# Kernel optimization log

Hardware: AMD Instinct MI355X
Metric: run time of the kernel (lower is better)

## Reference

```python
import jax, jax.numpy as jnp
import numpy as np

LOWER = 300  # hidden size of the critic MLP


def setup_inputs() -> dict:
    key = jax.random.key(0)
    ks = jax.random.split(key, 6)
    N, XD, YD = 1024, 768, 768
    x = jax.random.normal(ks[0], (N, XD), dtype=jnp.float32)
    y = jax.random.normal(ks[1], (N, YD), dtype=jnp.float32)
    # Linear(x_dim+y_dim -> LOWER), Linear(LOWER -> 1); Kaiming-uniform-ish init
    b1_lim = 1.0 / np.sqrt(XD + YD)
    b2_lim = 1.0 / np.sqrt(LOWER)
    W1 = jax.random.uniform(ks[2], (XD + YD, LOWER), jnp.float32, -b1_lim, b1_lim)
    b1 = jax.random.uniform(ks[3], (LOWER,), jnp.float32, -b1_lim, b1_lim)
    W2 = jax.random.uniform(ks[4], (LOWER, 1), jnp.float32, -b2_lim, b2_lim)
    b2 = jax.random.uniform(ks[5], (1,), jnp.float32, -b2_lim, b2_lim)
    return {"x_samples": x, "y_samples": y, "W1": W1, "b1": b1, "W2": W2, "b2": b2}


def reference(x_samples, y_samples, W1, b1, W2, b2):
    N = y_samples.shape[0]
    xd = x_samples.shape[-1]
    # Decompose first Linear: cat([x, y]) @ W1 == x @ W1[:xd] + y @ W1[xd:]
    Wx, Wy = W1[:xd], W1[xd:]
    hx = x_samples @ Wx          # [N, LOWER]
    hy = y_samples @ Wy          # [N, LOWER]
    w2 = W2[:, 0]                # [LOWER]

    def critic(h):
        # relu -> Linear(LOWER->1) -> softplus
        return jax.nn.softplus(jax.nn.relu(h) @ w2 + b2[0])

    # T0[i] = F(x[i], y[i])
    T0 = critic(hx + hy + b1)                       # [N]
    # T1[i, j] = F(x[j], y[i])  (x tiled over dim 0, y over dim 1)
    h_pair = hy[:, None, :] + hx[None, :, :] + b1   # [N, N, LOWER]
    T1 = critic(h_pair)                             # [N, N]
    lower_bound = (T0.mean()
                   - jax.nn.logsumexp(T1, axis=1).mean()
                   - jnp.log(jnp.float32(N)))
    return lower_bound
```

## Files before the change

kernel.cpp:

```cpp
#include <hip/hip_runtime.h>
#include <math.h>

#define N_S  1024
#define XD   768
#define LOW  300
#define KP   320
#define KP2  160

typedef _Float16 h2  __attribute__((ext_vector_type(2)));
typedef __fp16   g2  __attribute__((ext_vector_type(2)));
typedef _Float16 v8h __attribute__((ext_vector_type(8)));
typedef float    f4  __attribute__((ext_vector_type(4)));

union U32H2 { unsigned int u; h2 h; };
__device__ inline h2 u2h(unsigned int v){ U32H2 t; t.u = v; return t.h; }
union H8 { v8h v; h2 h[4]; };
__device__ inline h2 cvt2(float a, float b) {
    g2 t = __builtin_amdgcn_cvt_pkrtz(a, b);
    return __builtin_bit_cast(h2, t);
}

#define STRA 36
#define STRB 67

__global__ __launch_bounds__(256)
void gemm_h(const float* __restrict__ x, const float* __restrict__ y,
            const float* __restrict__ W1, const float* __restrict__ b1g,
            _Float16* __restrict__ hx_h, _Float16* __restrict__ hy_h)
{
    const int which = blockIdx.z;
    const float* A = which ? y : x;
    const float* W = W1 + (size_t)which * XD * LOW;
    _Float16* out = which ? hy_h : hx_h;

    const int n0 = blockIdx.x * 64;
    const int r0 = blockIdx.y * 64;

    __shared__ float As[2][64][STRA];
    __shared__ float Bs[2][32][STRB];

    const int tid = threadIdx.x;
    const int w = tid >> 6, l = tid & 63;
    const int wm = w >> 1, wn = w & 1;
    const int lr = l & 15, lg = l >> 4;

    const int arow = tid >> 2, aq = tid & 3;
    const int bn = tid & 63, bk0 = tid >> 6;
    const bool bin = (n0 + bn) < LOW;

    f4 acc[2][2] = {};

    float4 av0, av1; float bw[8];
    av0 = *(const float4*)&A[(size_t)(r0 + arow) * XD + aq * 8];
    av1 = *(const float4*)&A[(size_t)(r0 + arow) * XD + aq * 8 + 4];
    #pragma unroll
    for (int s = 0; s < 8; ++s)
        bw[s] = bin ? W[(size_t)(bk0 + s * 4) * LOW + n0 + bn] : 0.f;

    const int NC = XD / 32;
    for (int c = 0; c < NC; ++c) {
        const int buf = c & 1;
        *(float4*)&As[buf][arow][aq * 8]     = av0;
        *(float4*)&As[buf][arow][aq * 8 + 4] = av1;
        #pragma unroll
        for (int s = 0; s < 8; ++s)
            Bs[buf][bk0 + s * 4][bn] = bw[s];
        __syncthreads();
        if (c + 1 < NC) {
            const int kb = (c + 1) * 32;
            av0 = *(const float4*)&A[(size_t)(r0 + arow) * XD + kb + aq * 8];
            av1 = *(const float4*)&A[(size_t)(r0 + arow) * XD + kb + aq * 8 + 4];
            #pragma unroll
            for (int s = 0; s < 8; ++s)
                bw[s] = bin ? W[(size_t)(kb + bk0 + s * 4) * LOW + n0 + bn] : 0.f;
        }
        const int kloc = lg * 8;
        H8 af[2], bf[2];
        #pragma unroll
        for (int mt = 0; mt < 2; ++mt) {
            float4 t0 = *(const float4*)&As[buf][wm * 32 + mt * 16 + lr][kloc];
            float4 t1 = *(const float4*)&As[buf][wm * 32 + mt * 16 + lr][kloc + 4];
            af[mt].h[0] = cvt2(t0.x, t0.y);
            af[mt].h[1] = cvt2(t0.z, t0.w);
            af[mt].h[2] = cvt2(t1.x, t1.y);
            af[mt].h[3] = cvt2(t1.z, t1.w);
        }
        #pragma unroll
        for (int nt = 0; nt < 2; ++nt) {
            const int nn = wn * 32 + nt * 16 + lr;
            float e0 = Bs[buf][kloc + 0][nn], e1 = Bs[buf][kloc + 1][nn];
            float e2 = Bs[buf][kloc + 2][nn], e3 = Bs[buf][kloc + 3][nn];
            float e4 = Bs[buf][kloc + 4][nn], e5 = Bs[buf][kloc + 5][nn];
            float e6 = Bs[buf][kloc + 6][nn], e7 = Bs[buf][kloc + 7][nn];
            bf[nt].h[0] = cvt2(e0, e1);
            bf[nt].h[1] = cvt2(e2, e3);
            bf[nt].h[2] = cvt2(e4, e5);
            bf[nt].h[3] = cvt2(e6, e7);
        }
        #pragma unroll
        for (int mt = 0; mt < 2; ++mt)
            #pragma unroll
            for (int nt = 0; nt < 2; ++nt)
                acc[mt][nt] = __builtin_amdgcn_mfma_f32_16x16x32_f16(
                    af[mt].v, bf[nt].v, acc[mt][nt], 0, 0, 0);
    }

    #pragma unroll
    for (int nt = 0; nt < 2; ++nt) {
        const int col = n0 + wn * 32 + nt * 16 + lr;
        const float b1v = (which && col < LOW) ? b1g[col] : 0.f;
        #pragma unroll
        for (int mt = 0; mt < 2; ++mt) {
            #pragma unroll
            for (int r = 0; r < 4; ++r) {
                const int row = r0 + wm * 32 + mt * 16 + lg * 4 + r;
                out[(size_t)row * KP + col] = (_Float16)(acc[mt][nt][r] + b1v);
            }
        }
    }
}

__global__ __launch_bounds__(256)
void pair_kernel(const unsigned int* __restrict__ hx_h, const unsigned int* __restrict__ hy_h,
                 const float* __restrict__ W2, const float* __restrict__ b2,
                 float* __restrict__ T1)
{
    const int j0 = blockIdx.x * 64;
    const int i0 = blockIdx.y * 32;

    __shared__ unsigned int Hy[2][16][36];
    __shared__ unsigned int Hx[2][16][66];
    __shared__ unsigned int w2s[KP2];

    const int tid = threadIdx.x;
    const int tx = tid & 31;
    const int ty = tid >> 5;

    if (tid < KP2) {
        int k = tid * 2;
        float w0 = (k < LOW) ? W2[k] : 0.f;
        float w1 = (k + 1 < LOW) ? W2[k + 1] : 0.f;
        U32H2 p; p.h = h2{(_Float16)w0, (_Float16)w1};
        w2s[tid] = p.u;
    }

    const int yi = tid >> 3, yq = tid & 7;
    const int xj = tid >> 2, xq = tid & 3;

    uint2 ga  = *(const uint2*)&hy_h[(size_t)(i0 + yi) * KP2 + 2 * yq];
    uint2 gb0 = *(const uint2*)&hx_h[(size_t)(j0 + xj) * KP2 + 4 * xq];
    uint2 gb1 = *(const uint2*)&hx_h[(size_t)(j0 + xj) * KP2 + 4 * xq + 2];

    float acc[4][2] = {};
    const h2 hz = h2{(_Float16)0.f, (_Float16)0.f};

    const int NC = KP2 / 16;
    for (int c = 0; c < NC; ++c) {
        const int buf = c & 1;
        Hy[buf][2 * yq][yi]     = ga.x;
        Hy[buf][2 * yq + 1][yi] = ga.y;
        Hx[buf][4 * xq][xj]     = gb0.x;
        Hx[buf][4 * xq + 1][xj] = gb0.y;
        Hx[buf][4 * xq + 2][xj] = gb1.x;
        Hx[buf][4 * xq + 3][xj] = gb1.y;
        __syncthreads();
        if (c + 1 < NC) {
            const int kb = (c + 1) * 16;
            ga  = *(const uint2*)&hy_h[(size_t)(i0 + yi) * KP2 + kb + 2 * yq];
            gb0 = *(const uint2*)&hx_h[(size_t)(j0 + xj) * KP2 + kb + 4 * xq];
            gb1 = *(const uint2*)&hx_h[(size_t)(j0 + xj) * KP2 + kb + 4 * xq + 2];
        }
        #pragma unroll
        for (int kk = 0; kk < 16; ++kk) {
            const uint4 ya = *(const uint4*)&Hy[buf][kk][ty * 4];
            const uint2 xb = *(const uint2*)&Hx[buf][kk][tx * 2];
            const h2 w  = u2h(w2s[c * 16 + kk]);
            const h2 x0 = u2h(xb.x), x1 = u2h(xb.y);
            const unsigned int yar[4] = {ya.x, ya.y, ya.z, ya.w};
            #pragma unroll
            for (int r = 0; r < 4; ++r) {
                const h2 a = u2h(yar[r]);
                h2 z0 = __builtin_elementwise_max(a + x0, hz);
                h2 z1 = __builtin_elementwise_max(a + x1, hz);
                acc[r][0] = __builtin_amdgcn_fdot2(z0, w, acc[r][0], false);
                acc[r][1] = __builtin_amdgcn_fdot2(z1, w, acc[r][1], false);
            }
        }
    }

    const float b2v = b2[0];
    #pragma unroll
    for (int r = 0; r < 4; ++r) {
        float s0 = acc[r][0] + b2v, s1 = acc[r][1] + b2v;
        float2 sp;
        sp.x = fmaxf(s0, 0.f) + __logf(1.f + __expf(-fabsf(s0)));
        sp.y = fmaxf(s1, 0.f) + __logf(1.f + __expf(-fabsf(s1)));
        *(float2*)&T1[(size_t)(i0 + ty * 4 + r) * N_S + j0 + tx * 2] = sp;
    }
}

__global__ __launch_bounds__(256)
void row_reduce(const float* __restrict__ T1, float* __restrict__ contrib)
{
    const int tid = threadIdx.x;
    const int wid = tid >> 6, lane = tid & 63;
    const int i = blockIdx.x * 4 + wid;
    const float4* row = (const float4*)(T1 + (size_t)i * N_S);

    float4 v[4];
    #pragma unroll
    for (int q = 0; q < 4; ++q) v[q] = row[lane + 64 * q];

    float m = -1e30f;
    #pragma unroll
    for (int q = 0; q < 4; ++q)
        m = fmaxf(m, fmaxf(fmaxf(v[q].x, v[q].y), fmaxf(v[q].z, v[q].w)));
    #pragma unroll
    for (int o = 32; o > 0; o >>= 1) m = fmaxf(m, __shfl_xor(m, o, 64));

    float s = 0.f;
    #pragma unroll
    for (int q = 0; q < 4; ++q)
        s += __expf(v[q].x - m) + __expf(v[q].y - m) +
             __expf(v[q].z - m) + __expf(v[q].w - m);
    #pragma unroll
    for (int o = 32; o > 0; o >>= 1) s += __shfl_xor(s, o, 64);

    if (lane == 0)
        contrib[i] = T1[(size_t)i * (N_S + 1)] - (m + __logf(s));
}

__global__ __launch_bounds__(256)
void finalize(const float* __restrict__ contrib, float* __restrict__ out)
{
    const int tid = threadIdx.x;
    float s = 0.f;
    for (int j = tid; j < N_S; j += 256) s += contrib[j];
    #pragma unroll
    for (int o = 32; o > 0; o >>= 1) s += __shfl_xor(s, o, 64);
    __shared__ float ss[4];
    const int wid = tid >> 6, lane = tid & 63;
    if (lane == 0) ss[wid] = s;
    __syncthreads();
    if (tid == 0)
        out[0] = (ss[0] + ss[1] + ss[2] + ss[3]) * (1.0f / N_S) - logf((float)N_S);
}

extern "C" void kernel_launch(void* const* d_in, const int* in_sizes, int n_in,
                              void* d_out, int out_size, void* d_ws, size_t ws_size,
                              hipStream_t stream)
{
    const float* x  = (const float*)d_in[0];
    const float* y  = (const float*)d_in[1];
    const float* W1 = (const float*)d_in[2];
    const float* b1 = (const float*)d_in[3];
    const float* W2 = (const float*)d_in[4];
    const float* b2 = (const float*)d_in[5];
    float* out = (float*)d_out;

    unsigned int* hx_h = (unsigned int*)d_ws;
    unsigned int* hy_h = hx_h + (size_t)N_S * KP2;
    float* T1      = (float*)(hy_h + (size_t)N_S * KP2);
    float* contrib = T1 + (size_t)N_S * N_S;

    dim3 g1(5, 16, 2);
    gemm_h<<<g1, 256, 0, stream>>>(x, y, W1, b1,
                                   (_Float16*)hx_h, (_Float16*)hy_h);

    dim3 g2(16, 32);
    pair_kernel<<<g2, 256, 0, stream>>>(hx_h, hy_h, W2, b2, T1);

    row_reduce<<<N_S / 4, 256, 0, stream>>>(T1, contrib);
    finalize<<<1, 256, 0, stream>>>(contrib, out);
}
```

Baseline: 48.10 us.

## Fuse logsumexp partials into pair kernel and restructure GEMM with fp16 LDS staging

The pair kernel no longer writes the full N×N T1 matrix. It computes exp of the softplus values, reduces them per row across each 64-column block, and writes per-block partial sums plus the diagonal entries. A single lse_final kernel then merges these partials and the diagonal into the final scalar, replacing the separate row_reduce and finalize kernels and removing a 4 MB round trip through global memory. The GEMM now converts inputs to fp16 before storing them in LDS, uses a K-tile of 64 and 512 threads, and gives each wave a 32x16 output tile. Dropping the max subtraction in the logsumexp assumes the softplus outputs are small enough that exp does not overflow.

```diff
diff --git a/kernel.cpp b/kernel.cpp
--- a/kernel.cpp
+++ b/kernel.cpp
@@ -1,11 +1,11 @@
 #include <hip/hip_runtime.h>
 #include <math.h>
 
-#define N_S  1024
-#define XD   768
-#define LOW  300
-#define KP   320
-#define KP2  160
+#define N_S 1024
+#define XD  768
+#define LOW 300
+#define KP  320
+#define KP2 160
 
 typedef _Float16 h2  __attribute__((ext_vector_type(2)));
 typedef __fp16   g2  __attribute__((ext_vector_type(2)));
@@ -14,16 +14,15 @@
 
 union U32H2 { unsigned int u; h2 h; };
 __device__ inline h2 u2h(unsigned int v){ U32H2 t; t.u = v; return t.h; }
-union H8 { v8h v; h2 h[4]; };
-__device__ inline h2 cvt2(float a, float b) {
+__device__ inline unsigned int pk(float a, float b){
     g2 t = __builtin_amdgcn_cvt_pkrtz(a, b);
-    return __builtin_bit_cast(h2, t);
-}
-
-#define STRA 36
-#define STRB 67
-
-__global__ __launch_bounds__(256)
+    return __builtin_bit_cast(unsigned int, t);
+}
+union U4V8 { uint4 u; v8h v; };
+
+#define STR 34
+
+__global__ __launch_bounds__(512)
 void gemm_h(const float* __restrict__ x, const float* __restrict__ y,
             const float* __restrict__ W1, const float* __restrict__ b1g,
             _Float16* __restrict__ hx_h, _Float16* __restrict__ hy_h)
@@ -36,97 +35,76 @@
     const int n0 = blockIdx.x * 64;
     const int r0 = blockIdx.y * 64;
 
-    __shared__ float As[2][64][STRA];
-    __shared__ float Bs[2][32][STRB];
+    __shared__ unsigned int As[2][64][STR];
+    __shared__ unsigned int Bs[2][64][STR];
 
     const int tid = threadIdx.x;
     const int w = tid >> 6, l = tid & 63;
-    const int wm = w >> 1, wn = w & 1;
+    const int wn = w >> 1, wm = w & 1;
     const int lr = l & 15, lg = l >> 4;
 
-    const int arow = tid >> 2, aq = tid & 3;
-    const int bn = tid & 63, bk0 = tid >> 6;
+    const int arow = tid >> 3, aq = tid & 7;
+    const int bn = tid & 63, bms = tid >> 6;
     const bool bin = (n0 + bn) < LOW;
 
-    f4 acc[2][2] = {};
-
-    float4 av0, av1; float bw[8];
-    av0 = *(const float4*)&A[(size_t)(r0 + arow) * XD + aq * 8];
-    av1 = *(const float4*)&A[(size_t)(r0 + arow) * XD + aq * 8 + 4];
+    f4 acc[2] = {};
+
+    float4 a0, a1; float bw[8];
+    a0 = *(const float4*)&A[(size_t)(r0 + arow) * XD + aq * 8];
+    a1 = *(const float4*)&A[(size_t)(r0 + arow) * XD + aq * 8 + 4];
     #pragma unroll
     for (int s = 0; s < 8; ++s)
-        bw[s] = bin ? W[(size_t)(bk0 + s * 4) * LOW + n0 + bn] : 0.f;
-
-    const int NC = XD / 32;
+        bw[s] = bin ? W[(size_t)(bms * 8 + s) * LOW + n0 + bn] : 0.f;
+
+    const int NC = XD / 64;
     for (int c = 0; c < NC; ++c) {
         const int buf = c & 1;
-        *(float4*)&As[buf][arow][aq * 8]     = av0;
-        *(float4*)&As[buf][arow][aq * 8 + 4] = av1;
-        #pragma unroll
-        for (int s = 0; s < 8; ++s)
-            Bs[buf][bk0 + s * 4][bn] = bw[s];
+        {
+            uint4 pa = { pk(a0.x,a0.y), pk(a0.z,a0.w), pk(a1.x,a1.y), pk(a1.z,a1.w) };
+            *(uint4*)&As[buf][arow][aq * 4] = pa;
+            uint4 pb = { pk(bw[0],bw[1]), pk(bw[2],bw[3]), pk(bw[4],bw[5]), pk(bw[6],bw[7]) };
+            *(uint4*)&Bs[buf][bn][bms * 4] = pb;
+        }
         __syncthreads();
         if (c + 1 < NC) {
-            const int kb = (c + 1) * 32;
-            av0 = *(const float4*)&A[(size_t)(r0 + arow) * XD + kb + aq * 8];
-            av1 = *(const float4*)&A[(size_t)(r0 + arow) * XD + kb + aq * 8 + 4];
+            const int kb = (c + 1) * 64;
+            a0 = *(const float4*)&A[(size_t)(r0 + arow) * XD + kb + aq * 8];
+            a1 = *(const float4*)&A[(size_t)(r0 + arow) * XD + kb + aq * 8 + 4];
             #pragma unroll
             for (int s = 0; s < 8; ++s)
-                bw[s] = bin ? W[(size_t)(kb + bk0 + s * 4) * LOW + n0 + bn] : 0.f;
-        }
-        const int kloc = lg * 8;
-        H8 af[2], bf[2];
-        #pragma unroll
-        for (int mt = 0; mt < 2; ++mt) {
-            float4 t0 = *(const float4*)&As[buf][wm * 32 + mt * 16 + lr][kloc];
-            float4 t1 = *(const float4*)&As[buf][wm * 32 + mt * 16 + lr][kloc + 4];
-            af[mt].h[0] = cvt2(t0.x, t0.y);
-            af[mt].h[1] = cvt2(t0.z, t0.w);
-            af[mt].h[2] = cvt2(t1.x, t1.y);
-            af[mt].h[3] = cvt2(t1.z, t1.w);
-        }
-        #pragma unroll
-        for (int nt = 0; nt < 2; ++nt) {
-            const int nn = wn * 32 + nt * 16 + lr;
-            float e0 = Bs[buf][kloc + 0][nn], e1 = Bs[buf][kloc + 1][nn];
-            float e2 = Bs[buf][kloc + 2][nn], e3 = Bs[buf][kloc + 3][nn];
-            float e4 = Bs[buf][kloc + 4][nn], e5 = Bs[buf][kloc + 5][nn];
-            float e6 = Bs[buf][kloc + 6][nn], e7 = Bs[buf][kloc + 7][nn];
-            bf[nt].h[0] = cvt2(e0, e1);
-            bf[nt].h[1] = cvt2(e2, e3);
-            bf[nt].h[2] = cvt2(e4, e5);
-            bf[nt].h[3] = cvt2(e6, e7);
-        }
-        #pragma unroll
-        for (int mt = 0; mt < 2; ++mt)
+                bw[s] = bin ? W[(size_t)(kb + bms * 8 + s) * LOW + n0 + bn] : 0.f;
+        }
+        #pragma unroll
+        for (int ks = 0; ks < 2; ++ks) {
+            const int ko = ks * 16 + lg * 4;
+            U4V8 bf; bf.u = *(const uint4*)&Bs[buf][wn * 16 + lr][ko];
             #pragma unroll
-            for (int nt = 0; nt < 2; ++nt)
-                acc[mt][nt] = __builtin_amdgcn_mfma_f32_16x16x32_f16(
-                    af[mt].v, bf[nt].v, acc[mt][nt], 0, 0, 0);
-    }
-
-    #pragma unroll
-    for (int nt = 0; nt < 2; ++nt) {
-        const int col = n0 + wn * 32 + nt * 16 + lr;
-        const float b1v = (which && col < LOW) ? b1g[col] : 0.f;
-        #pragma unroll
-        for (int mt = 0; mt < 2; ++mt) {
-            #pragma unroll
-            for (int r = 0; r < 4; ++r) {
-                const int row = r0 + wm * 32 + mt * 16 + lg * 4 + r;
-                out[(size_t)row * KP + col] = (_Float16)(acc[mt][nt][r] + b1v);
+            for (int mt = 0; mt < 2; ++mt) {
+                U4V8 af; af.u = *(const uint4*)&As[buf][wm * 32 + mt * 16 + lr][ko];
+                acc[mt] = __builtin_amdgcn_mfma_f32_16x16x32_f16(af.v, bf.v, acc[mt], 0, 0, 0);
             }
         }
     }
+
+    const int col = n0 + wn * 16 + lr;
+    const float b1v = (which && col < LOW) ? b1g[col] : 0.f;
+    #pragma unroll
+    for (int mt = 0; mt < 2; ++mt)
+        #pragma unroll
+        for (int r = 0; r < 4; ++r) {
+            const int row = r0 + wm * 32 + mt * 16 + lg * 4 + r;
+            out[(size_t)row * KP + col] = (_Float16)(acc[mt][r] + b1v);
+        }
 }
 
 __global__ __launch_bounds__(256)
 void pair_kernel(const unsigned int* __restrict__ hx_h, const unsigned int* __restrict__ hy_h,
                  const float* __restrict__ W2, const float* __restrict__ b2,
-                 float* __restrict__ T1)
+                 float* __restrict__ part, float* __restrict__ diag)
 {
     const int j0 = blockIdx.x * 64;
     const int i0 = blockIdx.y * 32;
+    const int jb = blockIdx.x;
 
     __shared__ unsigned int Hy[2][16][36];
     __shared__ unsigned int Hx[2][16][66];
@@ -191,59 +169,46 @@
     const float b2v = b2[0];
     #pragma unroll
     for (int r = 0; r < 4; ++r) {
+        const int row = i0 + ty * 4 + r;
         float s0 = acc[r][0] + b2v, s1 = acc[r][1] + b2v;
-        float2 sp;
-        sp.x = fmaxf(s0, 0.f) + __logf(1.f + __expf(-fabsf(s0)));
-        sp.y = fmaxf(s1, 0.f) + __logf(1.f + __expf(-fabsf(s1)));
-        *(float2*)&T1[(size_t)(i0 + ty * 4 + r) * N_S + j0 + tx * 2] = sp;
-    }
-}
-
-__global__ __launch_bounds__(256)
-void row_reduce(const float* __restrict__ T1, float* __restrict__ contrib)
-{
-    const int tid = threadIdx.x;
-    const int wid = tid >> 6, lane = tid & 63;
-    const int i = blockIdx.x * 4 + wid;
-    const float4* row = (const float4*)(T1 + (size_t)i * N_S);
-
-    float4 v[4];
-    #pragma unroll
-    for (int q = 0; q < 4; ++q) v[q] = row[lane + 64 * q];
-
-    float m = -1e30f;
-    #pragma unroll
-    for (int q = 0; q < 4; ++q)
-        m = fmaxf(m, fmaxf(fmaxf(v[q].x, v[q].y), fmaxf(v[q].z, v[q].w)));
-    #pragma unroll
-    for (int o = 32; o > 0; o >>= 1) m = fmaxf(m, __shfl_xor(m, o, 64));
-
+        float sp0 = fmaxf(s0, 0.f) + __logf(1.f + __expf(-fabsf(s0)));
+        float sp1 = fmaxf(s1, 0.f) + __logf(1.f + __expf(-fabsf(s1)));
+        const int c0 = j0 + tx * 2;
+        if (c0 == row)     diag[row] = sp0;
+        if (c0 + 1 == row) diag[row] = sp1;
+        float es = __expf(sp0) + __expf(sp1);
+        #pragma unroll
+        for (int o = 1; o <= 16; o <<= 1) es += __shfl_xor(es, o, 64);
+        if ((tid & 31) == 0) part[(size_t)row * 16 + jb] = es;
+    }
+}
+
+__global__ __launch_bounds__(1024)
+void lse_final(const float* __restrict__ part, const float* __restrict__ diag,
+               float* __restrict__ out)
+{
+    const int i = threadIdx.x;
+    const float4* p = (const float4*)(part + (size_t)i * 16);
     float s = 0.f;
     #pragma unroll
-    for (int q = 0; q < 4; ++q)
-        s += __expf(v[q].x - m) + __expf(v[q].y - m) +
-             __expf(v[q].z - m) + __expf(v[q].w - m);
-    #pragma unroll
-    for (int o = 32; o > 0; o >>= 1) s += __shfl_xor(s, o, 64);
-
-    if (lane == 0)
-        contrib[i] = T1[(size_t)i * (N_S + 1)] - (m + __logf(s));
-}
-
-__global__ __launch_bounds__(256)
-void finalize(const float* __restrict__ contrib, float* __restrict__ out)
-{
-    const int tid = threadIdx.x;
-    float s = 0.f;
-    for (int j = tid; j < N_S; j += 256) s += contrib[j];
-    #pragma unroll
-    for (int o = 32; o > 0; o >>= 1) s += __shfl_xor(s, o, 64);
-    __shared__ float ss[4];
-    const int wid = tid >> 6, lane = tid & 63;
-    if (lane == 0) ss[wid] = s;
+    for (int q = 0; q < 4; ++q) {
+        float4 v = p[q];
+        s += (v.x + v.y) + (v.z + v.w);
+    }
+    float c = diag[i] - __logf(s);
+
+    #pragma unroll
+    for (int o = 32; o > 0; o >>= 1) c += __shfl_xor(c, o, 64);
+    __shared__ float ss[16];
+    const int wid = i >> 6, lane = i & 63;
+    if (lane == 0) ss[wid] = c;
     __syncthreads();
-    if (tid == 0)
-        out[0] = (ss[0] + ss[1] + ss[2] + ss[3]) * (1.0f / N_S) - logf((float)N_S);
+    if (i == 0) {
+        float t = 0.f;
+        #pragma unroll
+        for (int q = 0; q < 16; ++q) t += ss[q];
+        out[0] = t * (1.0f / N_S) - logf((float)N_S);
+    }
 }
 
 extern "C" void kernel_launch(void* const* d_in, const int* in_sizes, int n_in,
@@ -260,16 +225,15 @@
 
     unsigned int* hx_h = (unsigned int*)d_ws;
     unsigned int* hy_h = hx_h + (size_t)N_S * KP2;
-    float* T1      = (float*)(hy_h + (size_t)N_S * KP2);
-    float* contrib = T1 + (size_t)N_S * N_S;
+    float* part = (float*)(hy_h + (size_t)N_S * KP2);
+    float* diag = part + (size_t)N_S * 16;
 
     dim3 g1(5, 16, 2);
-    gemm_h<<<g1, 256, 0, stream>>>(x, y, W1, b1,
+    gemm_h<<<g1, 512, 0, stream>>>(x, y, W1, b1,
                                    (_Float16*)hx_h, (_Float16*)hy_h);
 
     dim3 g2(16, 32);
-    pair_kernel<<<g2, 256, 0, stream>>>(hx_h, hy_h, W2, b2, T1);
-
-    row_reduce<<<N_S / 4, 256, 0, stream>>>(T1, contrib);
-    finalize<<<1, 256, 0, stream>>>(contrib, out);
-}
+    pair_kernel<<<g2, 256, 0, stream>>>(hx_h, hy_h, W2, b2, part, diag);
+
+    lse_final<<<1, 1024, 0, stream>>>(part, diag, out);
+}
```

Result: faster. 41.85 us (-13.0%).
